# Performance work log

Hardware: AMD Instinct MI355X
Metric: run time of the kernel (lower is better)

The kernel has to match this reference:

```python
import jax, jax.numpy as jnp
import numpy as np

HEADS = 16
HEAD_DIM = 64
HIDDEN = HEADS * HEAD_DIM          # 1024
EXP = 4
QKVFF = HIDDEN * (3 + EXP)         # 7168
VFF = HIDDEN * (1 + EXP)           # 5120
B, L = 2, 2048
LN_EPS = 1e-5


def setup_inputs() -> dict:
    key = jax.random.key(0)
    k1, k2, k3 = jax.random.split(key, 3)
    x = jax.random.normal(k1, (B, L, HIDDEN), dtype=jnp.float32)
    W_in = jax.random.normal(k2, (HIDDEN, QKVFF), dtype=jnp.float32) * (HIDDEN ** -0.5)
    W_out = jax.random.normal(k3, (VFF, HIDDEN), dtype=jnp.float32) * (VFF ** -0.5)
    ln_w = jnp.ones((HIDDEN,), dtype=jnp.float32)
    ln_b = jnp.zeros((HIDDEN,), dtype=jnp.float32)
    return {"x": x, "ln_w": ln_w, "ln_b": ln_b, "W_in": W_in, "W_out": W_out}


def _rotary_tables(l, dtype):
    inv_freq = 1.0 / (10000.0 ** (jnp.arange(0, HEAD_DIM, 2, dtype=jnp.float32) / HEAD_DIM))
    t = jnp.arange(l, dtype=jnp.float32)
    freqs = t[:, None] * inv_freq[None, :]            # [l, d/2]
    emb = jnp.concatenate([freqs, freqs], axis=-1)     # [l, d]
    return jnp.cos(emb).astype(dtype), jnp.sin(emb).astype(dtype)


def _rotate_half(x):
    x1, x2 = jnp.split(x, 2, axis=-1)
    return jnp.concatenate([-x2, x1], axis=-1)


def reference(x, ln_w, ln_b, W_in, W_out):
    b, l, d = x.shape
    # shared LayerNorm
    mu = jnp.mean(x, axis=-1, keepdims=True)
    var = jnp.var(x, axis=-1, keepdims=True)
    xn = (x - mu) * jax.lax.rsqrt(var + LN_EPS) * ln_w + ln_b
    # fused in-projection
    h = xn @ W_in                                      # [b, l, qkvff]
    q, k, v, ff = jnp.split(h, [HIDDEN, 2 * HIDDEN, 3 * HIDDEN], axis=-1)
    q = q.reshape(b, l, HEADS, HEAD_DIM)
    k = k.reshape(b, l, HEADS, HEAD_DIM)
    v = v.reshape(b, l, HEADS, HEAD_DIM)
    # inline RoPE on q, k
    cos, sin = _rotary_tables(l, x.dtype)              # [l, d]
    cos = cos[None, :, None, :]
    sin = sin[None, :, None, :]
    q = q * cos + _rotate_half(q) * sin
    k = k * cos + _rotate_half(k) * sin
    # causal attention with explicit mask bias (as in the original)
    a = jnp.einsum('bihd,bjhd->bhij', q, k) * (HEAD_DIM ** -0.5)
    causal = jnp.tril(jnp.ones((l, l), dtype=a.dtype))
    a = a + (-1e10) * (1.0 - causal)
    a = jax.nn.softmax(a, axis=-1)
    o = jnp.einsum('bhij,bjhd->bihd', a, v).reshape(b, l, HIDDEN)
    # parallel FF branch
    ff = jax.nn.gelu(ff, approximate=False)
    return jnp.concatenate([o, ff], axis=-1) @ W_out
```

## Files before the change

### kernel.cpp

```cpp
#include <hip/hip_runtime.h>
#include <math.h>

#define HEADS 16
#define HEAD_DIM 64
#define HIDDEN 1024
#define NQKVFF 7168
#define VFF 5120
#define SEQ 2048
#define MROWS 4096

typedef unsigned short u16;
typedef __attribute__((ext_vector_type(8))) short bf16x8;
typedef __attribute__((ext_vector_type(4))) float f32x4;
typedef __attribute__((address_space(1))) void gas_void;
typedef __attribute__((address_space(3))) void las_void;

__device__ inline u16 f2bf(float f) {
    union { float f; unsigned u; } v; v.f = f;
    unsigned r = v.u + 0x7FFFu + ((v.u >> 16) & 1u);
    return (u16)(r >> 16);
}
__device__ inline float bf2f(u16 h) {
    union { unsigned u; float f; } v; v.u = ((unsigned)h) << 16;
    return v.f;
}

__global__ __launch_bounds__(256) void ln_kernel(const float* __restrict__ x,
        const float* __restrict__ w, const float* __restrict__ b,
        u16* __restrict__ xn) {
    int row = blockIdx.x;
    int tid = threadIdx.x;
    const float* xr = x + (size_t)row * HIDDEN;
    float4 v = ((const float4*)xr)[tid];
    float s = v.x + v.y + v.z + v.w;
    float sq = v.x * v.x + v.y * v.y + v.z * v.z + v.w * v.w;
    for (int off = 32; off > 0; off >>= 1) {
        s += __shfl_down(s, off, 64);
        sq += __shfl_down(sq, off, 64);
    }
    __shared__ float ls[4], lsq[4];
    int wid = tid >> 6, lane = tid & 63;
    if (lane == 0) { ls[wid] = s; lsq[wid] = sq; }
    __syncthreads();
    float ts = ls[0] + ls[1] + ls[2] + ls[3];
    float tsq = lsq[0] + lsq[1] + lsq[2] + lsq[3];
    float mu = ts * (1.0f / HIDDEN);
    float var = tsq * (1.0f / HIDDEN) - mu * mu;
    float rstd = rsqrtf(var + 1e-5f);
    float4 wv = ((const float4*)w)[tid];
    float4 bv = ((const float4*)b)[tid];
    ushort4 o;
    o.x = f2bf((v.x - mu) * rstd * wv.x + bv.x);
    o.y = f2bf((v.y - mu) * rstd * wv.y + bv.y);
    o.z = f2bf((v.z - mu) * rstd * wv.z + bv.z);
    o.w = f2bf((v.w - mu) * rstd * wv.w + bv.w);
    ((ushort4*)(xn + (size_t)row * HIDDEN))[tid] = o;
}

__global__ __launch_bounds__(256) void transpose_f2b(const float* __restrict__ in,
        u16* __restrict__ out, int R, int C) {
    __shared__ u16 tile[32][33];
    int c0 = blockIdx.x * 32, r0 = blockIdx.y * 32;
    int tx = threadIdx.x & 31, ty = threadIdx.x >> 5;
#pragma unroll
    for (int k = 0; k < 4; k++)
        tile[ty + k * 8][tx] = f2bf(in[(size_t)(r0 + ty + k * 8) * C + c0 + tx]);
    __syncthreads();
#pragma unroll
    for (int k = 0; k < 4; k++)
        out[(size_t)(c0 + ty + k * 8) * R + r0 + tx] = tile[tx][ty + k * 8];
}

__device__ inline void gemm_core_128(const u16* __restrict__ A, int lda,
                                     const u16* __restrict__ BT, int ldb,
                                     int Klen, int bm, int bn, f32x4 acc[4][4],
                                     u16* ldsA, u16* ldsB) {
    const int tid = threadIdx.x;
    const int wid = tid >> 6;
    const int lane = tid & 63;
    const int quad = lane >> 4;
    const int cc = lane & 15;
    const int wm = (wid >> 1) * 64;
    const int wn = (wid & 1) * 64;
#pragma unroll
    for (int i = 0; i < 4; i++)
#pragma unroll
        for (int j = 0; j < 4; j++)
#pragma unroll
            for (int r = 0; r < 4; r++) acc[i][j][r] = 0.0f;

    const int row = tid >> 2;
    const int gch = ((tid & 3) ^ ((row >> 1) & 3)) * 8;
    const int slot = (quad ^ ((cc >> 1) & 3)) * 8;
    for (int k0 = 0; k0 < Klen; k0 += 32) {
        __syncthreads();
#pragma unroll
        for (int I = 0; I < 2; I++) {
            int r128 = I * 64 + row;
            const u16* ga = A + (size_t)(bm + r128) * lda + k0 + gch;
            u16* la = ldsA + ((size_t)(I * 256 + (tid & 192))) * 8;
            __builtin_amdgcn_global_load_lds((gas_void*)ga, (las_void*)la, 16, 0, 0);
            const u16* gb = BT + (size_t)(bn + r128) * ldb + k0 + gch;
            u16* lb = ldsB + ((size_t)(I * 256 + (tid & 192))) * 8;
            __builtin_amdgcn_global_load_lds((gas_void*)gb, (las_void*)lb, 16, 0, 0);
        }
        __syncthreads();
        bf16x8 af[4], bfr[4];
#pragma unroll
        for (int t = 0; t < 4; t++) {
            af[t]  = *(const bf16x8*)(ldsA + (wm + t * 16 + cc) * 32 + slot);
            bfr[t] = *(const bf16x8*)(ldsB + (wn + t * 16 + cc) * 32 + slot);
        }
#pragma unroll
        for (int i = 0; i < 4; i++)
#pragma unroll
            for (int j = 0; j < 4; j++)
                acc[i][j] = __builtin_amdgcn_mfma_f32_16x16x32_bf16(af[i], bfr[j], acc[i][j], 0, 0, 0);
    }
}

__device__ inline float gelu_f(float v) {
    float u = v * (v * v * 0.044715f + 1.0f) * 0.7978845608028654f;
    u = fminf(u, 15.0f);
    float e = exp2f(u * 2.8853900817779268f);
    return v * (e / (e + 1.0f));
}

__global__ __launch_bounds__(256) void gemm1(const u16* __restrict__ xn,
        const u16* __restrict__ WinT, u16* __restrict__ qkb,
        u16* __restrict__ vtb, u16* __restrict__ a2) {
    __shared__ u16 ldsA[128 * 32];
    __shared__ u16 ldsB[128 * 32];
    int bm = blockIdx.x * 128, bn = blockIdx.y * 128;
    f32x4 acc[4][4];
    gemm_core_128(xn, HIDDEN, WinT, HIDDEN, HIDDEN, bm, bn, acc, ldsA, ldsB);
    const int tid = threadIdx.x, wid = tid >> 6, lane = tid & 63;
    const int quad = lane >> 4, cc = lane & 15;
    const int wm = (wid >> 1) * 64, wn = (wid & 1) * 64;
    const int m0 = bm + wm;
    const int b = m0 >> 11;

    if (bn >= 3072) {
#pragma unroll
        for (int i = 0; i < 4; i++)
#pragma unroll
            for (int j = 0; j < 4; j++)
#pragma unroll
                for (int r = 0; r < 4; r++) {
                    int m = m0 + i * 16 + quad * 4 + r;
                    int n = bn + wn + j * 16 + cc;
                    a2[(size_t)m * VFF + (n - 2048)] = f2bf(gelu_f(acc[i][j][r]));
                }
    } else if (bn >= 2048) {
        int hh = ((bn - 2048 + wn) >> 6) & 15;
        u16* dst = vtb + (size_t)(b * 16 + hh) * (HEAD_DIM * SEQ);
#pragma unroll
        for (int i = 0; i < 4; i++) {
            int key0 = (m0 + i * 16 + quad * 4) & 2047;
            size_t ob = (size_t)(key0 >> 5) * 2048 +
                        (((key0 & 31) >> 3) * 16 + cc) * 8 + (key0 & 7);
#pragma unroll
            for (int jf = 0; jf < 4; jf++) {
                ushort4 o;
                o.x = f2bf(acc[i][jf][0]);
                o.y = f2bf(acc[i][jf][1]);
                o.z = f2bf(acc[i][jf][2]);
                o.w = f2bf(acc[i][jf][3]);
                *(ushort4*)(dst + ob + jf * 512) = o;
            }
        }
    } else {
        int t = bn >> 10;
        int hh = ((bn + wn) >> 6) & 15;
        u16* base = qkb + (size_t)(t * 32 + b * 16 + hh) * (SEQ * HEAD_DIM);
        float scale = t ? 1.0f : 0.18033688011112043f;
        float f0 = expf(cc * -0.28782313662425572f);
        float f1 = expf((16 + cc) * -0.28782313662425572f);
        const int o0 = ((cc >> 3) * 16) * 8 + (cc & 7);
        const int o1 = ((2 + (cc >> 3)) * 16) * 8 + (cc & 7);
#pragma unroll
        for (int i = 0; i < 4; i++)
#pragma unroll
            for (int r = 0; r < 4; r++) {
                int pos = (m0 + i * 16 + quad * 4 + r) & 2047;
                int ob = (pos >> 4) * 1024 + (pos & 15) * 8;
                float s_, c_;
                __sincosf(pos * f0, &s_, &c_);
                float x1 = acc[i][0][r], x2 = acc[i][2][r];
                base[ob + o0]       = f2bf((x1 * c_ - x2 * s_) * scale);
                base[ob + o0 + 512] = f2bf((x2 * c_ + x1 * s_) * scale);
                __sincosf(pos * f1, &s_, &c_);
                x1 = acc[i][1][r]; x2 = acc[i][3][r];
                base[ob + o1]       = f2bf((x1 * c_ - x2 * s_) * scale);
                base[ob + o1 + 512] = f2bf((x2 * c_ + x1 * s_) * scale);
            }
    }
}

__global__ __launch_bounds__(256) void gemm2(const u16* __restrict__ a2,
        const u16* __restrict__ WoutT, float* __restrict__ p0, float* __restrict__ p1) {
    __shared__ u16 ldsA[128 * 32];
    __shared__ u16 ldsB[128 * 32];
    int bm = blockIdx.x * 128, bn = blockIdx.y * 128;
    int split = blockIdx.z;
    float* dst = split ? p1 : p0;
    f32x4 acc[4][4];
    gemm_core_128(a2 + split * 2560, VFF, WoutT + split * 2560, VFF, 2560,
                  bm, bn, acc, ldsA, ldsB);
    const int tid = threadIdx.x, wid = tid >> 6, lane = tid & 63;
    const int quad = lane >> 4, cc = lane & 15;
    const int wm = (wid >> 1) * 64, wn = (wid & 1) * 64;
#pragma unroll
    for (int i = 0; i < 4; i++)
#pragma unroll
        for (int j = 0; j < 4; j++)
#pragma unroll
            for (int r = 0; r < 4; r++) {
                int m = bm + wm + i * 16 + quad * 4 + r;
                int n = bn + wn + j * 16 + cc;
                dst[(size_t)m * HIDDEN + n] = acc[i][j][r];
            }
}

__global__ __launch_bounds__(256) void reduce2(const float* __restrict__ p0,
        const float* __restrict__ p1, float* __restrict__ out) {
    int i = blockIdx.x * 256 + threadIdx.x;
    float4 a = ((const float4*)p0)[i];
    float4 b = ((const float4*)p1)[i];
    a.x += b.x; a.y += b.y; a.z += b.z; a.w += b.w;
    ((float4*)out)[i] = a;
}

__global__ __launch_bounds__(256) void attn_kernel(const u16* __restrict__ qk,
        const u16* __restrict__ vt, u16* __restrict__ a2) {
    const int id  = blockIdx.x;
    const int bh  = (id & 7) * 4 + ((id >> 3) & 3);
    const int bx  = id >> 5;
    const int tid = threadIdx.x;
    const int wid = tid >> 6;
    const int lane = tid & 63;
    const int quad = lane >> 4;
    const int cc = lane & 15;
    const int slot = wid >> 1;
    const int parity = wid & 1;
    const int tile = slot ? (127 - bx) : bx;
    const int q0 = tile * 16;

    const u16* Qp = qk + (size_t)bh * (SEQ * HEAD_DIM);
    const u16* Kp = qk + (size_t)(32 + bh) * (SEQ * HEAD_DIM);
    const u16* VP = vt + (size_t)bh * (HEAD_DIM * SEQ);

    __shared__ u16 Pbuf[4][16 * 72];
    __shared__ float obuf[2][64 * 17];
    __shared__ float lbuf[2][16];
    u16* P = Pbuf[wid];

    const int bb = bh >> 4, hh = bh & 15;
    const int qcol = q0 + cc;

    bf16x8 qa0 = *(const bf16x8*)(Qp + (q0 >> 4) * 1024 + lane * 8);
    bf16x8 qa1 = *(const bf16x8*)(Qp + (q0 >> 4) * 1024 + 512 + lane * 8);

    float ps = 0.0f;
    f32x4 ot[4];
#pragma unroll
    for (int mt = 0; mt < 4; mt++)
#pragma unroll
        for (int r = 0; r < 4; r++) ot[mt][r] = 0.0f;

    for (int kb = parity * 64; kb < q0 + 16; kb += 128) {
        const bool diag = (kb + 64 > q0);
        f32x4 s[4];
        __builtin_amdgcn_s_setprio(1);
#pragma unroll
        for (int c = 0; c < 4; c++) {
            s[c][0] = -32.0f; s[c][1] = -32.0f; s[c][2] = -32.0f; s[c][3] = -32.0f;
            const u16* kblob = Kp + ((kb >> 4) + c) * 1024 + lane * 8;
            bf16x8 ka0 = *(const bf16x8*)(kblob);
            bf16x8 ka1 = *(const bf16x8*)(kblob + 512);
            s[c] = __builtin_amdgcn_mfma_f32_16x16x32_bf16(ka0, qa0, s[c], 0, 0, 0);
            s[c] = __builtin_amdgcn_mfma_f32_16x16x32_bf16(ka1, qa1, s[c], 0, 0, 0);
        }
        __builtin_amdgcn_s_setprio(0);
        bf16x8 vf[2][4];
#pragma unroll
        for (int kc = 0; kc < 2; kc++)
#pragma unroll
            for (int mt = 0; mt < 4; mt++)
                vf[kc][mt] = *(const bf16x8*)(VP + ((kb >> 5) + kc) * 2048 + mt * 512 + lane * 8);
        if (diag) {
#pragma unroll
            for (int c = 0; c < 4; c++)
#pragma unroll
                for (int r = 0; r < 4; r++) {
                    int key = kb + c * 16 + quad * 4 + r;
                    s[c][r] = (key <= qcol) ? s[c][r] : -10000.0f;
                }
        }
#pragma unroll
        for (int c = 0; c < 4; c++) {
            float p0v = exp2f(s[c][0]); ps += p0v;
            float p1v = exp2f(s[c][1]); ps += p1v;
            float p2v = exp2f(s[c][2]); ps += p2v;
            float p3v = exp2f(s[c][3]); ps += p3v;
            unsigned r0, r1;
            asm("v_cvt_pk_bf16_f32 %0, %1, %2" : "=v"(r0) : "v"(p0v), "v"(p1v));
            asm("v_cvt_pk_bf16_f32 %0, %1, %2" : "=v"(r1) : "v"(p2v), "v"(p3v));
            uint2 pk; pk.x = r0; pk.y = r1;
            *(uint2*)(P + cc * 72 + c * 16 + quad * 4) = pk;
        }
        asm volatile("s_waitcnt lgkmcnt(0)" ::: "memory");
        __builtin_amdgcn_s_setprio(1);
#pragma unroll
        for (int kc = 0; kc < 2; kc++) {
            bf16x8 pb = *(const bf16x8*)(P + cc * 72 + kc * 32 + quad * 8);
#pragma unroll
            for (int mt = 0; mt < 4; mt++)
                ot[mt] = __builtin_amdgcn_mfma_f32_16x16x32_bf16(vf[kc][mt], pb, ot[mt], 0, 0, 0);
        }
        __builtin_amdgcn_s_setprio(0);
    }

    ps += __shfl_xor(ps, 16, 64);
    ps += __shfl_xor(ps, 32, 64);

    if (parity == 1) {
        if (quad == 0) lbuf[slot][cc] = ps;
        float* ob = obuf[slot] + lane * 17;
#pragma unroll
        for (int mt = 0; mt < 4; mt++)
#pragma unroll
            for (int r = 0; r < 4; r++) ob[mt * 4 + r] = ot[mt][r];
    }
    __syncthreads();
    if (parity == 0) {
        float l = ps + lbuf[slot][cc];
        float rl = 1.0f / l;
        const float* ob = obuf[slot] + lane * 17;
        u16* dst = a2 + ((size_t)(bb * SEQ + q0 + cc)) * VFF + hh * 64;
#pragma unroll
        for (int mt = 0; mt < 4; mt++) {
            ushort4 o;
            o.x = f2bf((ot[mt][0] + ob[mt * 4 + 0]) * rl);
            o.y = f2bf((ot[mt][1] + ob[mt * 4 + 1]) * rl);
            o.z = f2bf((ot[mt][2] + ob[mt * 4 + 2]) * rl);
            o.w = f2bf((ot[mt][3] + ob[mt * 4 + 3]) * rl);
            *(ushort4*)(dst + mt * 16 + quad * 4) = o;
        }
    }
}

extern "C" void kernel_launch(void* const* d_in, const int* in_sizes, int n_in,
                              void* d_out, int out_size, void* d_ws, size_t ws_size,
                              hipStream_t stream) {
    const float* x     = (const float*)d_in[0];
    const float* ln_w  = (const float*)d_in[1];
    const float* ln_b  = (const float*)d_in[2];
    const float* W_in  = (const float*)d_in[3];
    const float* W_out = (const float*)d_in[4];
    float* out = (float*)d_out;
    char* ws = (char*)d_ws;
    u16* xn    = (u16*)(ws);
    u16* WinT  = (u16*)(ws + 8388608);
    u16* qkb   = (u16*)(ws + 23068672);
    u16* vtb   = (u16*)(ws + 39845888);
    u16* WoutT = (u16*)(ws + 48234496);
    u16* a2    = (u16*)(ws + 58720256);
    float* p0  = (float*)(ws);
    float* p1  = (float*)(ws + 16777216);

    ln_kernel<<<dim3(MROWS), dim3(256), 0, stream>>>(x, ln_w, ln_b, xn);
    transpose_f2b<<<dim3(NQKVFF / 32, HIDDEN / 32), dim3(256), 0, stream>>>(W_in, WinT, HIDDEN, NQKVFF);
    transpose_f2b<<<dim3(HIDDEN / 32, VFF / 32), dim3(256), 0, stream>>>(W_out, WoutT, VFF, HIDDEN);
    gemm1<<<dim3(MROWS / 128, NQKVFF / 128), dim3(256), 0, stream>>>(xn, WinT, qkb, vtb, a2);
    attn_kernel<<<dim3(2048), dim3(256), 0, stream>>>(qkb, vtb, a2);
    gemm2<<<dim3(MROWS / 128, HIDDEN / 128, 2), dim3(256), 0, stream>>>(a2, WoutT, p0, p1);
    reduce2<<<dim3(MROWS * HIDDEN / 4 / 256), dim3(256), 0, stream>>>(p0, p1, out);
}
```

Baseline: 318.3 us.

## Double-buffer LDS tiles in the shared GEMM core to overlap loads with MFMA

The GEMM main loop now uses two LDS buffers. The next K-slice is issued with global_load_lds into the spare buffer while MFMAs run on the current one, which drops one barrier per iteration and hides global-load latency. Wave priority is raised around the MFMA block with s_setprio. LDS per block doubles to 32 KB, which may limit occupancy. Correctness depends on the barrier also waiting for outstanding direct-to-LDS loads.

```diff
diff --git a/kernel.cpp b/kernel.cpp
--- a/kernel.cpp
+++ b/kernel.cpp
@@ -74,7 +74,7 @@
 __device__ inline void gemm_core_128(const u16* __restrict__ A, int lda,
                                      const u16* __restrict__ BT, int ldb,
                                      int Klen, int bm, int bn, f32x4 acc[4][4],
-                                     u16* ldsA, u16* ldsB) {
+                                     u16* lds) {
     const int tid = threadIdx.x;
     const int wid = tid >> 6;
     const int lane = tid & 63;
@@ -92,30 +92,52 @@
     const int row = tid >> 2;
     const int gch = ((tid & 3) ^ ((row >> 1) & 3)) * 8;
     const int slot = (quad ^ ((cc >> 1) & 3)) * 8;
+    const int lofs = (tid & 192) * 8;
+
+    u16* cur = lds;
+    u16* nxt = lds + 8192;
+
+#pragma unroll
+    for (int I = 0; I < 2; I++) {
+        int r128 = I * 64 + row;
+        const u16* ga = A + (size_t)(bm + r128) * lda + gch;
+        __builtin_amdgcn_global_load_lds((gas_void*)ga,
+                (las_void*)(cur + I * 2048 + lofs), 16, 0, 0);
+        const u16* gb = BT + (size_t)(bn + r128) * ldb + gch;
+        __builtin_amdgcn_global_load_lds((gas_void*)gb,
+                (las_void*)(cur + 4096 + I * 2048 + lofs), 16, 0, 0);
+    }
+    __syncthreads();
+
     for (int k0 = 0; k0 < Klen; k0 += 32) {
-        __syncthreads();
-#pragma unroll
-        for (int I = 0; I < 2; I++) {
-            int r128 = I * 64 + row;
-            const u16* ga = A + (size_t)(bm + r128) * lda + k0 + gch;
-            u16* la = ldsA + ((size_t)(I * 256 + (tid & 192))) * 8;
-            __builtin_amdgcn_global_load_lds((gas_void*)ga, (las_void*)la, 16, 0, 0);
-            const u16* gb = BT + (size_t)(bn + r128) * ldb + k0 + gch;
-            u16* lb = ldsB + ((size_t)(I * 256 + (tid & 192))) * 8;
-            __builtin_amdgcn_global_load_lds((gas_void*)gb, (las_void*)lb, 16, 0, 0);
-        }
-        __syncthreads();
+        const bool more = (k0 + 32 < Klen);
+        if (more) {
+#pragma unroll
+            for (int I = 0; I < 2; I++) {
+                int r128 = I * 64 + row;
+                const u16* ga = A + (size_t)(bm + r128) * lda + k0 + 32 + gch;
+                __builtin_amdgcn_global_load_lds((gas_void*)ga,
+                        (las_void*)(nxt + I * 2048 + lofs), 16, 0, 0);
+                const u16* gb = BT + (size_t)(bn + r128) * ldb + k0 + 32 + gch;
+                __builtin_amdgcn_global_load_lds((gas_void*)gb,
+                        (las_void*)(nxt + 4096 + I * 2048 + lofs), 16, 0, 0);
+            }
+        }
         bf16x8 af[4], bfr[4];
 #pragma unroll
         for (int t = 0; t < 4; t++) {
-            af[t]  = *(const bf16x8*)(ldsA + (wm + t * 16 + cc) * 32 + slot);
-            bfr[t] = *(const bf16x8*)(ldsB + (wn + t * 16 + cc) * 32 + slot);
-        }
+            af[t]  = *(const bf16x8*)(cur + (wm + t * 16 + cc) * 32 + slot);
+            bfr[t] = *(const bf16x8*)(cur + 4096 + (wn + t * 16 + cc) * 32 + slot);
+        }
+        __builtin_amdgcn_s_setprio(1);
 #pragma unroll
         for (int i = 0; i < 4; i++)
 #pragma unroll
             for (int j = 0; j < 4; j++)
                 acc[i][j] = __builtin_amdgcn_mfma_f32_16x16x32_bf16(af[i], bfr[j], acc[i][j], 0, 0, 0);
+        __builtin_amdgcn_s_setprio(0);
+        if (more) __syncthreads();
+        u16* tmp = cur; cur = nxt; nxt = tmp;
     }
 }
 
@@ -129,11 +151,10 @@
 __global__ __launch_bounds__(256) void gemm1(const u16* __restrict__ xn,
         const u16* __restrict__ WinT, u16* __restrict__ qkb,
         u16* __restrict__ vtb, u16* __restrict__ a2) {
-    __shared__ u16 ldsA[128 * 32];
-    __shared__ u16 ldsB[128 * 32];
+    __shared__ u16 lds[2 * 8192];
     int bm = blockIdx.x * 128, bn = blockIdx.y * 128;
     f32x4 acc[4][4];
-    gemm_core_128(xn, HIDDEN, WinT, HIDDEN, HIDDEN, bm, bn, acc, ldsA, ldsB);
+    gemm_core_128(xn, HIDDEN, WinT, HIDDEN, HIDDEN, bm, bn, acc, lds);
     const int tid = threadIdx.x, wid = tid >> 6, lane = tid & 63;
     const int quad = lane >> 4, cc = lane & 15;
     const int wm = (wid >> 1) * 64, wn = (wid & 1) * 64;
@@ -199,14 +220,13 @@
 
 __global__ __launch_bounds__(256) void gemm2(const u16* __restrict__ a2,
         const u16* __restrict__ WoutT, float* __restrict__ p0, float* __restrict__ p1) {
-    __shared__ u16 ldsA[128 * 32];
-    __shared__ u16 ldsB[128 * 32];
+    __shared__ u16 lds[2 * 8192];
     int bm = blockIdx.x * 128, bn = blockIdx.y * 128;
     int split = blockIdx.z;
     float* dst = split ? p1 : p0;
     f32x4 acc[4][4];
     gemm_core_128(a2 + split * 2560, VFF, WoutT + split * 2560, VFF, 2560,
-                  bm, bn, acc, ldsA, ldsB);
+                  bm, bn, acc, lds);
     const int tid = threadIdx.x, wid = tid >> 6, lane = tid & 63;
     const int quad = lane >> 4, cc = lane & 15;
     const int wm = (wid >> 1) * 64, wn = (wid & 1) * 64;
```

Result: faster. 306.2 us (median of 2 runs) (-3.8%).

## Triple-buffer LDS tiles with two-deep async prefetch in GEMM core

Applied to the files above, without the earlier changes.

Replaces the single-buffered load/sync/compute loop in the shared GEMM core with a three-slot LDS ring. Tiles for k-steps t+1 and t+2 are fetched via global_load_lds while step t computes. Per-iteration synchronisation drops to one vmcnt-gated barrier, and MFMA blocks are wrapped in s_setprio to favour matrix issue. This hides global memory latency behind compute but triples LDS per block to 48KB, which may reduce occupancy.

```diff
diff --git a/kernel.cpp b/kernel.cpp
--- a/kernel.cpp
+++ b/kernel.cpp
@@ -71,10 +71,26 @@
         out[(size_t)(c0 + ty + k * 8) * R + r0 + tx] = tile[tx][ty + k * 8];
 }
 
+__device__ inline void stage_tile(const u16* __restrict__ A, int lda,
+                                  const u16* __restrict__ BT, int ldb,
+                                  int bm, int bn, int k0, u16* dst,
+                                  int row, int gch, int lofs) {
+#pragma unroll
+    for (int I = 0; I < 2; I++) {
+        int r128 = I * 64 + row;
+        const u16* ga = A + (size_t)(bm + r128) * lda + k0 + gch;
+        __builtin_amdgcn_global_load_lds((gas_void*)ga,
+                (las_void*)(dst + I * 2048 + lofs), 16, 0, 0);
+        const u16* gb = BT + (size_t)(bn + r128) * ldb + k0 + gch;
+        __builtin_amdgcn_global_load_lds((gas_void*)gb,
+                (las_void*)(dst + 4096 + I * 2048 + lofs), 16, 0, 0);
+    }
+}
+
 __device__ inline void gemm_core_128(const u16* __restrict__ A, int lda,
                                      const u16* __restrict__ BT, int ldb,
                                      int Klen, int bm, int bn, f32x4 acc[4][4],
-                                     u16* ldsA, u16* ldsB) {
+                                     u16* lds) {
     const int tid = threadIdx.x;
     const int wid = tid >> 6;
     const int lane = tid & 63;
@@ -92,30 +108,34 @@
     const int row = tid >> 2;
     const int gch = ((tid & 3) ^ ((row >> 1) & 3)) * 8;
     const int slot = (quad ^ ((cc >> 1) & 3)) * 8;
-    for (int k0 = 0; k0 < Klen; k0 += 32) {
-        __syncthreads();
-#pragma unroll
-        for (int I = 0; I < 2; I++) {
-            int r128 = I * 64 + row;
-            const u16* ga = A + (size_t)(bm + r128) * lda + k0 + gch;
-            u16* la = ldsA + ((size_t)(I * 256 + (tid & 192))) * 8;
-            __builtin_amdgcn_global_load_lds((gas_void*)ga, (las_void*)la, 16, 0, 0);
-            const u16* gb = BT + (size_t)(bn + r128) * ldb + k0 + gch;
-            u16* lb = ldsB + ((size_t)(I * 256 + (tid & 192))) * 8;
-            __builtin_amdgcn_global_load_lds((gas_void*)gb, (las_void*)lb, 16, 0, 0);
-        }
-        __syncthreads();
+    const int lofs = (tid & 192) * 8;
+
+    const int nt = Klen >> 5;
+    stage_tile(A, lda, BT, ldb, bm, bn, 0,  lds,        row, gch, lofs);
+    stage_tile(A, lda, BT, ldb, bm, bn, 32, lds + 8192, row, gch, lofs);
+
+    for (int t = 0; t < nt; ++t) {
+        if (t + 1 < nt)
+            asm volatile("s_waitcnt vmcnt(4)\n\ts_barrier" ::: "memory");
+        else
+            asm volatile("s_waitcnt vmcnt(0)\n\ts_barrier" ::: "memory");
+        u16* cur = lds + (unsigned)(t % 3) * 8192;
+        if (t + 2 < nt)
+            stage_tile(A, lda, BT, ldb, bm, bn, (t + 2) * 32,
+                       lds + (unsigned)((t + 2) % 3) * 8192, row, gch, lofs);
         bf16x8 af[4], bfr[4];
 #pragma unroll
-        for (int t = 0; t < 4; t++) {
-            af[t]  = *(const bf16x8*)(ldsA + (wm + t * 16 + cc) * 32 + slot);
-            bfr[t] = *(const bf16x8*)(ldsB + (wn + t * 16 + cc) * 32 + slot);
-        }
+        for (int u = 0; u < 4; u++) {
+            af[u]  = *(const bf16x8*)(cur + (wm + u * 16 + cc) * 32 + slot);
+            bfr[u] = *(const bf16x8*)(cur + 4096 + (wn + u * 16 + cc) * 32 + slot);
+        }
+        __builtin_amdgcn_s_setprio(1);
 #pragma unroll
         for (int i = 0; i < 4; i++)
 #pragma unroll
             for (int j = 0; j < 4; j++)
                 acc[i][j] = __builtin_amdgcn_mfma_f32_16x16x32_bf16(af[i], bfr[j], acc[i][j], 0, 0, 0);
+        __builtin_amdgcn_s_setprio(0);
     }
 }
 
@@ -129,11 +149,10 @@
 __global__ __launch_bounds__(256) void gemm1(const u16* __restrict__ xn,
         const u16* __restrict__ WinT, u16* __restrict__ qkb,
         u16* __restrict__ vtb, u16* __restrict__ a2) {
-    __shared__ u16 ldsA[128 * 32];
-    __shared__ u16 ldsB[128 * 32];
+    __shared__ u16 lds[3 * 8192];
     int bm = blockIdx.x * 128, bn = blockIdx.y * 128;
     f32x4 acc[4][4];
-    gemm_core_128(xn, HIDDEN, WinT, HIDDEN, HIDDEN, bm, bn, acc, ldsA, ldsB);
+    gemm_core_128(xn, HIDDEN, WinT, HIDDEN, HIDDEN, bm, bn, acc, lds);
     const int tid = threadIdx.x, wid = tid >> 6, lane = tid & 63;
     const int quad = lane >> 4, cc = lane & 15;
     const int wm = (wid >> 1) * 64, wn = (wid & 1) * 64;
@@ -199,14 +218,13 @@
 
 __global__ __launch_bounds__(256) void gemm2(const u16* __restrict__ a2,
         const u16* __restrict__ WoutT, float* __restrict__ p0, float* __restrict__ p1) {
-    __shared__ u16 ldsA[128 * 32];
-    __shared__ u16 ldsB[128 * 32];
+    __shared__ u16 lds[3 * 8192];
     int bm = blockIdx.x * 128, bn = blockIdx.y * 128;
     int split = blockIdx.z;
     float* dst = split ? p1 : p0;
     f32x4 acc[4][4];
     gemm_core_128(a2 + split * 2560, VFF, WoutT + split * 2560, VFF, 2560,
-                  bm, bn, acc, ldsA, ldsB);
+                  bm, bn, acc, lds);
     const int tid = threadIdx.x, wid = tid >> 6, lane = tid & 63;
     const int quad = lane >> 4, cc = lane & 15;
     const int wm = (wid >> 1) * 64, wn = (wid & 1) * 64;
```

Result: faster. 309.5 us (-2.7%).
